# Performance work log

Hardware: AMD Instinct MI355X
Metric: run time of the kernel (lower is better)

Reference implementation:

```python
import jax, jax.numpy as jnp
import numpy as np

MASK_VALUE = -1000000.0  # matches torch source's value=-1000000.0


def setup_inputs() -> dict:
    key = jax.random.key(0)
    kq, kk, kv, kl = jax.random.split(key, 4)
    B, S, D = 64, 1024, 64
    q = jax.random.normal(kq, (B, S, D), dtype=jnp.float32)
    k = jax.random.normal(kk, (B, S, D), dtype=jnp.float32)
    v = jax.random.normal(kv, (B, S, D), dtype=jnp.float32)
    valid_lens = jax.random.randint(kl, (B,), 0, S, dtype=jnp.int32)
    return {"q": q, "k": k, "v": v, "valid_lens": valid_lens}


def reference(q, k, v, valid_lens):
    # scores: [B, Sq, Sk]
    d = q.shape[-1]
    scores = jnp.einsum("bqd,bkd->bqk", q, k) / jnp.sqrt(jnp.float32(d))
    # 1-D valid_lens broadcast over the query dim (torch repeat_interleave branch)
    Sk = k.shape[1]
    mask = jnp.arange(Sk, dtype=jnp.int32)[None, None, :] < valid_lens[:, None, None]
    scores = jnp.where(mask, scores, MASK_VALUE)
    attn = jax.nn.softmax(scores, axis=-1)
    # dropout p=0.0 -> identity (eval-mode reference)
    return jnp.einsum("bqk,bkd->bqd", attn, v)
```

## Files before the change

kernel.cpp:

```cpp
#include <hip/hip_runtime.h>
#include <math.h>


#define BATCH 64
#define SEQ   1024
#define DIM   64
#define BQ    64
#define BC    64
#define NKT   (SEQ / BC)
#define LSTR  72
#define QSCALE 0.18033688011112442f
#define MASKED -1.0e6f

typedef __attribute__((ext_vector_type(8))) short bf16x8;
typedef __attribute__((ext_vector_type(4))) float f32x4;

__device__ __forceinline__ uint pack2_trunc(float lo, float hi) {
    return __builtin_amdgcn_perm(__float_as_uint(hi), __float_as_uint(lo), 0x07060302);
}
__device__ __forceinline__ ushort f2bf_rne(float x) {
    uint u = __float_as_uint(x);
    return (ushort)((u + 0x7fffu + ((u >> 16) & 1u)) >> 16);
}

__global__ __launch_bounds__(256, 4) void attn_mfma_flash3(
    const float* __restrict__ q, const float* __restrict__ k,
    const float* __restrict__ v, const int* __restrict__ valid_lens,
    float* __restrict__ out)
{
    __shared__ ushort Ks[BC * LSTR];
    __shared__ ushort Vt[DIM * LSTR];
    __shared__ ushort Ps[BQ * LSTR];

    const int t    = threadIdx.x;
    const int wave = t >> 6;
    const int wl   = t & 63;
    const int QD   = wl >> 4;
    const int li   = wl & 15;
    const int b    = blockIdx.x & 63;
    const int q0   = (blockIdx.x >> 6) * BQ;
    const int vl   = valid_lens[b];

    const size_t boff = (size_t)b * SEQ * DIM;

    bf16x8 qb[2];
    {
        const float* qrow = q + boff + (size_t)(q0 + wave * 16 + li) * DIM + QD * 8;
        #pragma unroll
        for (int kc = 0; kc < 2; kc++) {
            float4 a = *(const float4*)(qrow + kc * 32);
            float4 c = *(const float4*)(qrow + kc * 32 + 4);
            union { bf16x8 v; ushort u[8]; } tmp;
            tmp.u[0] = f2bf_rne(a.x * QSCALE);
            tmp.u[1] = f2bf_rne(a.y * QSCALE);
            tmp.u[2] = f2bf_rne(a.z * QSCALE);
            tmp.u[3] = f2bf_rne(a.w * QSCALE);
            tmp.u[4] = f2bf_rne(c.x * QSCALE);
            tmp.u[5] = f2bf_rne(c.y * QSCALE);
            tmp.u[6] = f2bf_rne(c.z * QSCALE);
            tmp.u[7] = f2bf_rne(c.w * QSCALE);
            qb[kc] = tmp.v;
        }
    }

    const int it_max = (vl == 0) ? NKT : ((vl + BC - 1) >> 6);

    float4 kf[4];
    float  vf[2][8];

    auto load_tile = [&](int it) {
        const float4* kg = (const float4*)(k + boff + (size_t)it * BC * DIM);
        #pragma unroll
        for (int i = 0; i < 4; i++) kf[i] = kg[t + 256 * i];
        const float* vgf = v + boff + (size_t)it * BC * DIM;
        #pragma unroll
        for (int i = 0; i < 2; i++) {
            int slot = t + 256 * i;
            int d = slot & 63, ko = slot >> 6;
            #pragma unroll
            for (int j = 0; j < 8; j++)
                vf[i][j] = vgf[(size_t)(ko * 8 + j) * DIM + d];
        }
    };

    auto stage = [&]() {
        #pragma unroll
        for (int i = 0; i < 4; i++) {
            int idx = t + 256 * i;
            int row = idx >> 4, c4 = idx & 15;
            uint2 w;
            w.x = pack2_trunc(kf[i].x, kf[i].y);
            w.y = pack2_trunc(kf[i].z, kf[i].w);
            *(uint2*)&Ks[row * LSTR + c4 * 4] = w;
        }
        #pragma unroll
        for (int i = 0; i < 2; i++) {
            int slot = t + 256 * i;
            int d = slot & 63, ko = slot >> 6;
            uint4 w;
            w.x = pack2_trunc(vf[i][0], vf[i][1]);
            w.y = pack2_trunc(vf[i][2], vf[i][3]);
            w.z = pack2_trunc(vf[i][4], vf[i][5]);
            w.w = pack2_trunc(vf[i][6], vf[i][7]);
            *(uint4*)&Vt[d * LSTR + ko * 8] = w;
        }
    };

    float m_run = -INFINITY, l_run = 0.f;
    f32x4 acc[4];
    #pragma unroll
    for (int dt = 0; dt < 4; dt++) acc[dt] = (f32x4){0.f, 0.f, 0.f, 0.f};

    load_tile(0);

    for (int it = 0; it < it_max; it++) {
        __builtin_amdgcn_sched_barrier(0);
        __builtin_amdgcn_s_barrier();
        __builtin_amdgcn_sched_barrier(0);

        stage();
        if (it + 1 < it_max) load_tile(it + 1);

        __builtin_amdgcn_sched_barrier(0);
        asm volatile("s_waitcnt lgkmcnt(0)" ::: "memory");
        __builtin_amdgcn_s_barrier();
        __builtin_amdgcn_sched_barrier(0);

        f32x4 sc[4];
        #pragma unroll
        for (int kt = 0; kt < 4; kt++) {
            bf16x8 ka0 = *(const bf16x8*)&Ks[(kt * 16 + li) * LSTR + QD * 8];
            bf16x8 ka1 = *(const bf16x8*)&Ks[(kt * 16 + li) * LSTR + 32 + QD * 8];
            f32x4 c = (f32x4){0.f, 0.f, 0.f, 0.f};
            c = __builtin_amdgcn_mfma_f32_16x16x32_bf16(ka0, qb[0], c, 0, 0, 0);
            c = __builtin_amdgcn_mfma_f32_16x16x32_bf16(ka1, qb[1], c, 0, 0, 0);
            sc[kt] = c;
        }

        const int kbase = it * BC;
        if (kbase + BC > vl) {
            #pragma unroll
            for (int kt = 0; kt < 4; kt++)
                #pragma unroll
                for (int r = 0; r < 4; r++) {
                    int key = kbase + kt * 16 + QD * 4 + r;
                    if (key >= vl) sc[kt][r] = MASKED;
                }
        }

        float mt = -INFINITY;
        #pragma unroll
        for (int kt = 0; kt < 4; kt++)
            #pragma unroll
            for (int r = 0; r < 4; r++) mt = fmaxf(mt, sc[kt][r]);
        mt = fmaxf(mt, __shfl_xor(mt, 16, 64));
        mt = fmaxf(mt, __shfl_xor(mt, 32, 64));
        float mn = fmaxf(m_run, mt);
        float alpha = exp2f(m_run - mn);
        m_run = mn;

        float ls = 0.f;
        #pragma unroll
        for (int kt = 0; kt < 4; kt++) {
            float p0 = exp2f(sc[kt][0] - mn);
            float p1 = exp2f(sc[kt][1] - mn);
            float p2 = exp2f(sc[kt][2] - mn);
            float p3 = exp2f(sc[kt][3] - mn);
            ls += (p0 + p1) + (p2 + p3);
            uint2 w;
            w.x = pack2_trunc(p0, p1);
            w.y = pack2_trunc(p2, p3);
            *(uint2*)&Ps[(wave * 16 + li) * LSTR + kt * 16 + QD * 4] = w;
        }
        ls += __shfl_xor(ls, 16, 64);
        ls += __shfl_xor(ls, 32, 64);
        l_run = l_run * alpha + ls;

        float a0 = __shfl(alpha, QD * 4 + 0, 64);
        float a1 = __shfl(alpha, QD * 4 + 1, 64);
        float a2 = __shfl(alpha, QD * 4 + 2, 64);
        float a3 = __shfl(alpha, QD * 4 + 3, 64);
        #pragma unroll
        for (int dt = 0; dt < 4; dt++) {
            acc[dt][0] *= a0; acc[dt][1] *= a1;
            acc[dt][2] *= a2; acc[dt][3] *= a3;
        }

        bf16x8 pa0 = *(const bf16x8*)&Ps[(wave * 16 + li) * LSTR + QD * 8];
        bf16x8 pa1 = *(const bf16x8*)&Ps[(wave * 16 + li) * LSTR + 32 + QD * 8];
        #pragma unroll
        for (int dt = 0; dt < 4; dt++) {
            bf16x8 vb0 = *(const bf16x8*)&Vt[(dt * 16 + li) * LSTR + QD * 8];
            bf16x8 vb1 = *(const bf16x8*)&Vt[(dt * 16 + li) * LSTR + 32 + QD * 8];
            acc[dt] = __builtin_amdgcn_mfma_f32_16x16x32_bf16(pa0, vb0, acc[dt], 0, 0, 0);
            acc[dt] = __builtin_amdgcn_mfma_f32_16x16x32_bf16(pa1, vb1, acc[dt], 0, 0, 0);
        }
    }

    float invl = 1.0f / l_run;
    float i0 = __shfl(invl, QD * 4 + 0, 64);
    float i1 = __shfl(invl, QD * 4 + 1, 64);
    float i2 = __shfl(invl, QD * 4 + 2, 64);
    float i3 = __shfl(invl, QD * 4 + 3, 64);
    float* ob = out + boff + (size_t)q0 * DIM;
    const int rbase = wave * 16 + QD * 4;
    #pragma unroll
    for (int dt = 0; dt < 4; dt++) {
        int col = dt * 16 + li;
        ob[(size_t)(rbase + 0) * DIM + col] = acc[dt][0] * i0;
        ob[(size_t)(rbase + 1) * DIM + col] = acc[dt][1] * i1;
        ob[(size_t)(rbase + 2) * DIM + col] = acc[dt][2] * i2;
        ob[(size_t)(rbase + 3) * DIM + col] = acc[dt][3] * i3;
    }
}

extern "C" void kernel_launch(void* const* d_in, const int* in_sizes, int n_in,
                              void* d_out, int out_size, void* d_ws, size_t ws_size,
                              hipStream_t stream) {
    const float* q = (const float*)d_in[0];
    const float* k = (const float*)d_in[1];
    const float* v = (const float*)d_in[2];
    const int* valid_lens = (const int*)d_in[3];
    float* out = (float*)d_out;

    dim3 grid(BATCH * (SEQ / BQ));
    dim3 block(256);
    attn_mfma_flash3<<<grid, block, 0, stream>>>(q, k, v, valid_lens, out);
}
```

Before: 127.9 us.

## Keep P in registers via permuted V staging and add lazy rescaling

Drops the shared-memory round trip for the softmax probabilities. The V tile is now staged with a permuted key order so the QK^T MFMA output layout can feed the PV MFMA directly from registers, which also frees the Ps LDS buffer. It also adds FA4-style lazy rescaling: the running max and the accumulator rescale are updated only when some row's new max exceeds the old one by more than a threshold. This removes LDS writes and reads plus per-tile rescale work, at the cost of more divergent control flow and unnormalised exponents that can reach up to 2^8.

```diff
diff --git a/kernel.cpp b/kernel.cpp
--- a/kernel.cpp
+++ b/kernel.cpp
@@ -11,6 +11,7 @@
 #define LSTR  72
 #define QSCALE 0.18033688011112442f
 #define MASKED -1.0e6f
+#define THR    8.0f
 
 typedef __attribute__((ext_vector_type(8))) short bf16x8;
 typedef __attribute__((ext_vector_type(4))) float f32x4;
@@ -23,14 +24,13 @@
     return (ushort)((u + 0x7fffu + ((u >> 16) & 1u)) >> 16);
 }
 
-__global__ __launch_bounds__(256, 4) void attn_mfma_flash3(
+__global__ __launch_bounds__(256, 4) void attn_mfma_flash4(
     const float* __restrict__ q, const float* __restrict__ k,
     const float* __restrict__ v, const int* __restrict__ valid_lens,
     float* __restrict__ out)
 {
     __shared__ ushort Ks[BC * LSTR];
     __shared__ ushort Vt[DIM * LSTR];
-    __shared__ ushort Ps[BQ * LSTR];
 
     const int t    = threadIdx.x;
     const int wave = t >> 6;
@@ -77,9 +77,12 @@
         for (int i = 0; i < 2; i++) {
             int slot = t + 256 * i;
             int d = slot & 63, ko = slot >> 6;
-            #pragma unroll
-            for (int j = 0; j < 8; j++)
-                vf[i][j] = vgf[(size_t)(ko * 8 + j) * DIM + d];
+            int kb = (ko >> 2) * 16 + (ko & 3) * 4;
+            #pragma unroll
+            for (int j = 0; j < 8; j++) {
+                int kk = kb + ((j >> 2) << 5) + (j & 3);
+                vf[i][j] = vgf[(size_t)kk * DIM + d];
+            }
         }
     };
 
@@ -155,45 +158,55 @@
             for (int r = 0; r < 4; r++) mt = fmaxf(mt, sc[kt][r]);
         mt = fmaxf(mt, __shfl_xor(mt, 16, 64));
         mt = fmaxf(mt, __shfl_xor(mt, 32, 64));
-        float mn = fmaxf(m_run, mt);
-        float alpha = exp2f(m_run - mn);
-        m_run = mn;
+
+        if (!__all(mt - m_run <= THR)) {
+            float mn = fmaxf(m_run, mt);
+            float alpha = exp2f(m_run - mn);
+            m_run = mn;
+            l_run *= alpha;
+            float a0 = __shfl(alpha, QD * 4 + 0, 64);
+            float a1 = __shfl(alpha, QD * 4 + 1, 64);
+            float a2 = __shfl(alpha, QD * 4 + 2, 64);
+            float a3 = __shfl(alpha, QD * 4 + 3, 64);
+            #pragma unroll
+            for (int dt = 0; dt < 4; dt++) {
+                acc[dt][0] *= a0; acc[dt][1] *= a1;
+                acc[dt][2] *= a2; acc[dt][3] *= a3;
+            }
+        }
 
         float ls = 0.f;
-        #pragma unroll
-        for (int kt = 0; kt < 4; kt++) {
-            float p0 = exp2f(sc[kt][0] - mn);
-            float p1 = exp2f(sc[kt][1] - mn);
-            float p2 = exp2f(sc[kt][2] - mn);
-            float p3 = exp2f(sc[kt][3] - mn);
-            ls += (p0 + p1) + (p2 + p3);
-            uint2 w;
-            w.x = pack2_trunc(p0, p1);
-            w.y = pack2_trunc(p2, p3);
-            *(uint2*)&Ps[(wave * 16 + li) * LSTR + kt * 16 + QD * 4] = w;
+        union { bf16x8 v; uint u[4]; } pa0u, pa1u;
+        {
+            float p00 = exp2f(sc[0][0] - m_run), p01 = exp2f(sc[0][1] - m_run);
+            float p02 = exp2f(sc[0][2] - m_run), p03 = exp2f(sc[0][3] - m_run);
+            float p10 = exp2f(sc[1][0] - m_run), p11 = exp2f(sc[1][1] - m_run);
+            float p12 = exp2f(sc[1][2] - m_run), p13 = exp2f(sc[1][3] - m_run);
+            float p20 = exp2f(sc[2][0] - m_run), p21 = exp2f(sc[2][1] - m_run);
+            float p22 = exp2f(sc[2][2] - m_run), p23 = exp2f(sc[2][3] - m_run);
+            float p30 = exp2f(sc[3][0] - m_run), p31 = exp2f(sc[3][1] - m_run);
+            float p32 = exp2f(sc[3][2] - m_run), p33 = exp2f(sc[3][3] - m_run);
+            ls = ((p00 + p01) + (p02 + p03)) + ((p10 + p11) + (p12 + p13))
+               + ((p20 + p21) + (p22 + p23)) + ((p30 + p31) + (p32 + p33));
+            pa0u.u[0] = pack2_trunc(p00, p01);
+            pa0u.u[1] = pack2_trunc(p02, p03);
+            pa0u.u[2] = pack2_trunc(p20, p21);
+            pa0u.u[3] = pack2_trunc(p22, p23);
+            pa1u.u[0] = pack2_trunc(p10, p11);
+            pa1u.u[1] = pack2_trunc(p12, p13);
+            pa1u.u[2] = pack2_trunc(p30, p31);
+            pa1u.u[3] = pack2_trunc(p32, p33);
         }
         ls += __shfl_xor(ls, 16, 64);
         ls += __shfl_xor(ls, 32, 64);
-        l_run = l_run * alpha + ls;
-
-        float a0 = __shfl(alpha, QD * 4 + 0, 64);
-        float a1 = __shfl(alpha, QD * 4 + 1, 64);
-        float a2 = __shfl(alpha, QD * 4 + 2, 64);
-        float a3 = __shfl(alpha, QD * 4 + 3, 64);
-        #pragma unroll
-        for (int dt = 0; dt < 4; dt++) {
-            acc[dt][0] *= a0; acc[dt][1] *= a1;
-            acc[dt][2] *= a2; acc[dt][3] *= a3;
-        }
-
-        bf16x8 pa0 = *(const bf16x8*)&Ps[(wave * 16 + li) * LSTR + QD * 8];
-        bf16x8 pa1 = *(const bf16x8*)&Ps[(wave * 16 + li) * LSTR + 32 + QD * 8];
+        l_run += ls;
+
         #pragma unroll
         for (int dt = 0; dt < 4; dt++) {
             bf16x8 vb0 = *(const bf16x8*)&Vt[(dt * 16 + li) * LSTR + QD * 8];
             bf16x8 vb1 = *(const bf16x8*)&Vt[(dt * 16 + li) * LSTR + 32 + QD * 8];
-            acc[dt] = __builtin_amdgcn_mfma_f32_16x16x32_bf16(pa0, vb0, acc[dt], 0, 0, 0);
-            acc[dt] = __builtin_amdgcn_mfma_f32_16x16x32_bf16(pa1, vb1, acc[dt], 0, 0, 0);
+            acc[dt] = __builtin_amdgcn_mfma_f32_16x16x32_bf16(pa0u.v, vb0, acc[dt], 0, 0, 0);
+            acc[dt] = __builtin_amdgcn_mfma_f32_16x16x32_bf16(pa1u.v, vb1, acc[dt], 0, 0, 0);
         }
     }
 
@@ -225,5 +238,5 @@
 
     dim3 grid(BATCH * (SEQ / BQ));
     dim3 block(256);
-    attn_mfma_flash3<<<grid, block, 0, stream>>>(q, k, v, valid_lens, out);
-}
+    attn_mfma_flash4<<<grid, block, 0, stream>>>(q, k, v, valid_lens, out);
+}
```

Measured after the change: 124.4 us. 1.03x faster.
